# Kernel optimization log

Hardware: AMD Instinct MI355X
Metric: run time of the kernel (lower is better)

Reference implementation:

```python
import jax, jax.numpy as jnp
import numpy as np

# dims: L = 1 + H*W tokens (cls first), BT = B*T clips*frames
L, BT, D = 577, 128, 768
B, T = 16, 8
H = W = 24
CM = 192   # d_middle = D // REDUCTION(4)
CR = 48    # CM // rf_r(4)
K = 3      # rf_k and spatial kernel


def setup_inputs() -> dict:
    key = jax.random.key(0)
    ks = jax.random.split(key, 10)
    return {
        "x":      jax.random.normal(ks[0], (L, BT, D), jnp.float32),
        # tada_pre_proj: Linear(D -> CM)
        "w_pre":  jax.random.normal(ks[1], (D, CM), jnp.float32) * 0.02,
        "b_pre":  jnp.zeros((CM,), jnp.float32),
        # TAdaConv2dV2 base depthwise weight (1x3x3, groups=CM) and bias
        "w_base": jax.random.normal(ks[2], (K, K, 1, CM), jnp.float32) * 0.1,
        "b_conv": jnp.zeros((CM,), jnp.float32),
        # route function: global 1x1 branch, temporal conv a (CM->CR), temporal conv b (CR->CM, small init)
        "w_g":    jax.random.normal(ks[3], (CM, CM), jnp.float32) * 0.02,
        "b_g":    jnp.zeros((CM,), jnp.float32),
        "w_a":    jax.random.normal(ks[4], (K, CM, CR), jnp.float32) * 0.05,
        "b_a":    jnp.zeros((CR,), jnp.float32),
        "w_b":    jax.random.normal(ks[5], (K, CR, CM), jnp.float32) * 0.02,
        # tada_proj: Linear(CM -> D)
        "w_proj": jax.random.normal(ks[6], (CM, D), jnp.float32) * 0.02,
        "b_proj": jnp.zeros((D,), jnp.float32),
    }


def reference(x, w_pre, b_pre, w_base, b_conv, w_g, b_g, w_a, b_a, w_b, w_proj, b_proj):
    # --- tada_pre_proj ---
    h = x @ w_pre + b_pre                                   # [L, BT, CM]
    cls_tok, sp = h[:1], h[1:]                              # cls token bypasses the conv
    sp = sp.transpose(1, 0, 2).reshape(BT, H, W, CM)        # [BT, H, W, CM]

    # --- route function: per-frame, per-channel calibration alpha ---
    d = sp.reshape(B, T, H * W, CM).mean(axis=2)            # spatial avg pool -> [B, T, CM]
    g = d.mean(axis=1) @ w_g + b_g                          # global temporal descriptor [B, CM]
    a = jax.lax.conv_general_dilated(d + g[:, None, :], w_a, (1,), 'SAME',
                                     dimension_numbers=('NWC', 'WIO', 'NWC')) + b_a
    a = jax.nn.relu(a)                                      # [B, T, CR]
    alpha = jax.lax.conv_general_dilated(a, w_b, (1,), 'SAME',
                                         dimension_numbers=('NWC', 'WIO', 'NWC')) + 1.0  # [B, T, CM]

    # --- calibrated depthwise conv (cal_dim='cout') ---
    # conv2d(x, alpha * W_base) == alpha * conv2d(x, W_base) for depthwise cout calibration
    y = jax.lax.conv_general_dilated(sp, w_base, (1, 1), 'SAME',
                                     dimension_numbers=('NHWC', 'HWIO', 'NHWC'),
                                     feature_group_count=CM)
    y = y * alpha.reshape(BT, 1, 1, CM) + b_conv            # [BT, H, W, CM]
    y = y.reshape(BT, H * W, CM).transpose(1, 0, 2)         # [HW, BT, CM]
    out = jnp.concatenate([cls_tok, y], axis=0)             # [L, BT, CM]

    # --- QuickGELU + tada_proj ---
    out = out * jax.nn.sigmoid(1.702 * out)
    return out @ w_proj + b_proj                            # [L, BT, D]
```

## Files before the change

kernel.cpp:

```cpp
#include <hip/hip_runtime.h>

#define DEV __device__ __forceinline__

typedef short bf16x8 __attribute__((ext_vector_type(8)));
typedef float f32x4  __attribute__((ext_vector_type(4)));
typedef unsigned short ushort_t;


DEV unsigned short f2bf(float f) {
  unsigned u = __float_as_uint(f);
  unsigned r = (u + 0x7fffu + ((u >> 16) & 1u)) >> 16;
  return (unsigned short)r;
}

DEV unsigned cvt_pk_bf16(float a, float b) {
  unsigned r;
  asm("v_cvt_pk_bf16_f32 %0, %1, %2" : "=v"(r) : "v"(a), "v"(b));
  return r;
}

DEV float bf2f(unsigned short b) { return __uint_as_float((unsigned)b << 16); }

DEV float silu_g(float v) { return v / (1.f + __expf(-1.702f * v)); }

DEV void gload_lds16(const void* g, void* l) {
  __builtin_amdgcn_global_load_lds(
      (const __attribute__((address_space(1))) unsigned int*)g,
      (__attribute__((address_space(3))) unsigned int*)l, 16, 0, 0);
}

__global__ __launch_bounds__(256)
void prep_kernel(const float* __restrict__ w_pre, const float* __restrict__ w_proj,
                 short* __restrict__ w_preT, short* __restrict__ w_projT) {
  int i = blockIdx.x * 256 + threadIdx.x;
  if (i < 192 * 768) {
    int n = i / 768, k = i - n * 768;
    w_preT[i] = (short)f2bf(w_pre[k * 192 + n]);
    int n2 = i / 192, k2 = i - n2 * 192;
    w_projT[i] = (short)f2bf(w_proj[k2 * 768 + n2]);
  }
}

__global__ __launch_bounds__(512, 4)
void gemm1_kernel(const float* __restrict__ Af, const short* __restrict__ Bt,
                  const float* __restrict__ bias, ushort_t* __restrict__ C) {
  constexpr int BM = 128, BK = 64, KTOT = 768, NTOT = 192, NT = 12;
  __shared__ short As[2][BM * BK];
  __shared__ short Bs[2][192 * BK];

  const int tid  = threadIdx.x;
  const int wave = tid >> 6, lane = tid & 63;
  const int m0 = blockIdx.x * BM;
  const int wm = wave >> 2, wn = wave & 3;
  const int lr  = lane & 15;
  const int lk8 = lane >> 4;
  const int srow = lane >> 3;
  const int schunk = lane & 7;

  f32x4 acc[4][3] = {};
  float4 areg[2][2];

  auto loadA_f32 = [&](int kt) {
    #pragma unroll
    for (int s = 0; s < 2; ++s) {
      int id = tid + s * 512;
      int r = id >> 3, c = id & 7;
      int cg = c ^ (r & 7);
      const float* p = Af + (size_t)(m0 + r) * KTOT + kt + cg * 8;
      areg[s][0] = *(const float4*)p;
      areg[s][1] = *(const float4*)(p + 4);
    }
  };
  auto cvtStoreA = [&](int buf) {
    #pragma unroll
    for (int s = 0; s < 2; ++s) {
      int id = tid + s * 512;
      int r = id >> 3, c = id & 7;
      int4 w;
      w.x = (int)cvt_pk_bf16(areg[s][0].x, areg[s][0].y);
      w.y = (int)cvt_pk_bf16(areg[s][0].z, areg[s][0].w);
      w.z = (int)cvt_pk_bf16(areg[s][1].x, areg[s][1].y);
      w.w = (int)cvt_pk_bf16(areg[s][1].z, areg[s][1].w);
      *(int4*)&As[buf][r * 64 + c * 8] = w;
    }
  };
  auto stageB = [&](int kt, int buf) {
    #pragma unroll
    for (int j = 0; j < 3; ++j) {
      int rb8 = wave * 3 + j;
      int r = rb8 * 8 + srow;
      const short* src = Bt + (size_t)r * KTOT + kt + (schunk ^ srow) * 8;
      gload_lds16(src, (char*)Bs[buf] + rb8 * 1024);
    }
  };
  auto compute = [&](int buf) {
    #pragma unroll
    for (int ks = 0; ks < 2; ++ks) {
      int kc = ks * 4 + lk8;
      bf16x8 af[4], bfv[3];
      #pragma unroll
      for (int fm = 0; fm < 4; ++fm) {
        int row = wm * 64 + fm * 16 + lr;
        af[fm] = *(const bf16x8*)&As[buf][row * 64 + (kc ^ (row & 7)) * 8];
      }
      #pragma unroll
      for (int fn = 0; fn < 3; ++fn) {
        int row = wn * 48 + fn * 16 + lr;
        bfv[fn] = *(const bf16x8*)&Bs[buf][row * 64 + (kc ^ (row & 7)) * 8];
      }
      #pragma unroll
      for (int fm = 0; fm < 4; ++fm)
        #pragma unroll
        for (int fn = 0; fn < 3; ++fn)
          acc[fm][fn] = __builtin_amdgcn_mfma_f32_16x16x32_bf16(
              bfv[fn], af[fm], acc[fm][fn], 0, 0, 0);
    }
  };

  loadA_f32(0);
  cvtStoreA(0);
  stageB(0, 0);
  loadA_f32(BK);
  asm volatile("s_waitcnt vmcnt(4) lgkmcnt(0)" ::: "memory");
  __builtin_amdgcn_s_barrier();

  #pragma unroll
  for (int t = 0; t < NT; ++t) {
    const int cur = t & 1, nxt = cur ^ 1;
    if (t + 1 < NT) {
      stageB((t + 1) * BK, nxt);
      cvtStoreA(nxt);
      if (t + 2 < NT) loadA_f32((t + 2) * BK);
    }
    compute(cur);
    if (t + 1 < NT) {
      if (t + 2 < NT)
        asm volatile("s_waitcnt vmcnt(4) lgkmcnt(0)" ::: "memory");
      else
        asm volatile("s_waitcnt vmcnt(0) lgkmcnt(0)" ::: "memory");
      __builtin_amdgcn_s_barrier();
    }
  }

  const int cb = (lane >> 4) * 4;
  #pragma unroll
  for (int fm = 0; fm < 4; ++fm) {
    int row = m0 + wm * 64 + fm * 16 + lr;
    #pragma unroll
    for (int fn = 0; fn < 3; ++fn) {
      int col = wn * 48 + fn * 16 + cb;
      float4 bv = *(const float4*)(bias + col);
      int2 w;
      w.x = (int)cvt_pk_bf16(acc[fm][fn][0] + bv.x, acc[fm][fn][1] + bv.y);
      w.y = (int)cvt_pk_bf16(acc[fm][fn][2] + bv.z, acc[fm][fn][3] + bv.w);
      *(int2*)&C[(size_t)row * NTOT + col] = w;
    }
  }
}

__global__ __launch_bounds__(384)
void reduce_d_kernel(const ushort_t* __restrict__ h, float* __restrict__ d) {
  const int bt = blockIdx.x, tid = threadIdx.x;
  const int slice = tid / 24, c8 = tid % 24;
  __shared__ float part[16][192];
  float sum[8] = {};
  #pragma unroll 4
  for (int i = 0; i < 36; ++i) {
    int l = 1 + slice * 36 + i;
    bf16x8 v = *(const bf16x8*)&h[((size_t)l * 128 + bt) * 192 + c8 * 8];
    #pragma unroll
    for (int j = 0; j < 8; ++j) sum[j] += bf2f((unsigned short)v[j]);
  }
  #pragma unroll
  for (int j = 0; j < 8; ++j) part[slice][c8 * 8 + j] = sum[j];
  __syncthreads();
  if (tid < 192) {
    float s = 0.f;
    #pragma unroll
    for (int sl = 0; sl < 16; ++sl) s += part[sl][tid];
    d[bt * 192 + tid] = s * (1.f / 576.f);
  }
}

__global__ __launch_bounds__(256)
void small_path_kernel(const float* __restrict__ d,
                       const float* __restrict__ w_g, const float* __restrict__ b_g,
                       const float* __restrict__ w_a, const float* __restrict__ b_a,
                       const float* __restrict__ w_b,
                       float* __restrict__ alpha) {
  const int b = blockIdx.x, tid = threadIdx.x;
  __shared__ unsigned short wg_buf[36864];
  __shared__ unsigned short wa_buf[27648];
  __shared__ float e[8][192];
  __shared__ float md[192];
  __shared__ float a[8][48];

  #pragma unroll
  for (int it = 0; it < 36; ++it) {
    int i = tid + it * 256;
    float4 v = *(const float4*)(w_g + i * 4);
    int2 w;
    w.x = (int)cvt_pk_bf16(v.x, v.y);
    w.y = (int)cvt_pk_bf16(v.z, v.w);
    *(int2*)&wg_buf[i * 4] = w;
  }
  #pragma unroll
  for (int it = 0; it < 27; ++it) {
    int i = tid + it * 256;
    float4 v = *(const float4*)(w_a + i * 4);
    int2 w;
    w.x = (int)cvt_pk_bf16(v.x, v.y);
    w.y = (int)cvt_pk_bf16(v.z, v.w);
    *(int2*)&wa_buf[i * 4] = w;
  }
  for (int i = tid; i < 384; i += 256)
    *(float4*)((float*)e + i * 4) = *(const float4*)(d + (size_t)b * 1536 + i * 4);
  __syncthreads();

  if (tid < 192) {
    float m = 0.f;
    #pragma unroll
    for (int t = 0; t < 8; ++t) m += e[t][tid];
    md[tid] = m * 0.125f;
  }
  __syncthreads();

  if (tid < 192) {
    float accg = b_g[tid];
    #pragma unroll 8
    for (int k = 0; k < 192; ++k)
      accg += md[k] * bf2f(wg_buf[k * 192 + tid]);
    #pragma unroll
    for (int t = 0; t < 8; ++t) e[t][tid] += accg;
  }
  __syncthreads();

  #pragma unroll
  for (int it = 0; it < 27; ++it) {
    int i = tid + it * 256;
    float4 v = *(const float4*)(w_b + i * 4);
    int2 w;
    w.x = (int)cvt_pk_bf16(v.x, v.y);
    w.y = (int)cvt_pk_bf16(v.z, v.w);
    *(int2*)&wg_buf[i * 4] = w;
  }
  for (int o = tid; o < 384; o += 256) {
    int t = o / 48, r = o - t * 48;
    float acc = b_a[r];
    #pragma unroll
    for (int dt = 0; dt < 3; ++dt) {
      int tt = t + dt - 1;
      if ((unsigned)tt < 8u) {
        #pragma unroll 8
        for (int k = 0; k < 192; ++k)
          acc += e[tt][k] * bf2f(wa_buf[(dt * 192 + k) * 48 + r]);
      }
    }
    a[t][r] = fmaxf(acc, 0.f);
  }
  __syncthreads();

  if (tid < 192) {
    #pragma unroll
    for (int t = 0; t < 8; ++t) {
      float acc = 1.0f;
      #pragma unroll
      for (int dt = 0; dt < 3; ++dt) {
        int tt = t + dt - 1;
        if ((unsigned)tt < 8u) {
          #pragma unroll 8
          for (int r = 0; r < 48; ++r)
            acc += a[tt][r] * bf2f(wg_buf[(dt * 48 + r) * 192 + tid]);
        }
      }
      alpha[(size_t)(b * 8 + t) * 192 + tid] = acc;
    }
  }
}

__global__ __launch_bounds__(512, 4)
void fused_out_kernel(const ushort_t* __restrict__ h, const float* __restrict__ alpha,
                      const float* __restrict__ w_base, const float* __restrict__ b_conv,
                      const short* __restrict__ Bt, const float* __restrict__ bias,
                      float* __restrict__ out) {
  constexpr int NTOT = 768;
  __shared__ ushort_t Stile[64 * 192];

  const int tid  = threadIdx.x;
  const int l    = blockIdx.x >> 1;
  const int bt0  = (blockIdx.x & 1) * 64;
  const int wave = tid >> 6, lane = tid & 63;
  const int wm = wave >> 2, wn = wave & 3;
  const int lr = lane & 15, lk8 = lane >> 4;

  const int row = tid >> 3;
  const int cg  = tid & 7;
  const int bt  = bt0 + row;
  if (l == 0) {
    #pragma unroll
    for (int j = 0; j < 3; ++j) {
      int c8 = cg + 8 * j;
      bf16x8 hv = *(const bf16x8*)&h[(size_t)bt * 192 + c8 * 8];
      float v0 = silu_g(bf2f((ushort_t)hv[0])), v1 = silu_g(bf2f((ushort_t)hv[1]));
      float v2 = silu_g(bf2f((ushort_t)hv[2])), v3 = silu_g(bf2f((ushort_t)hv[3]));
      float v4 = silu_g(bf2f((ushort_t)hv[4])), v5 = silu_g(bf2f((ushort_t)hv[5]));
      float v6 = silu_g(bf2f((ushort_t)hv[6])), v7 = silu_g(bf2f((ushort_t)hv[7]));
      int4 pk;
      pk.x = (int)cvt_pk_bf16(v0, v1); pk.y = (int)cvt_pk_bf16(v2, v3);
      pk.z = (int)cvt_pk_bf16(v4, v5); pk.w = (int)cvt_pk_bf16(v6, v7);
      int chp = (c8 & ~7) | ((c8 & 7) ^ (row & 7));
      *(int4*)&Stile[row * 192 + chp * 8] = pk;
    }
  } else {
    const int p = l - 1, hh = p / 24, ww = p - hh * 24;
    #pragma unroll
    for (int j = 0; j < 3; ++j) {
      int c8 = cg + 8 * j;
      int cbase = c8 * 8;
      float acc8[8] = {};
      #pragma unroll
      for (int dh = 0; dh < 3; ++dh) {
        int y = hh + dh - 1;
        if ((unsigned)y >= 24u) continue;
        #pragma unroll
        for (int dw = 0; dw < 3; ++dw) {
          int xx = ww + dw - 1;
          if ((unsigned)xx >= 24u) continue;
          bf16x8 hv = *(const bf16x8*)
              &h[((size_t)(1 + y * 24 + xx) * 128 + bt) * 192 + cbase];
          const float* wp = w_base + (dh * 3 + dw) * 192 + cbase;
          float4 w0 = *(const float4*)wp, w1 = *(const float4*)(wp + 4);
          acc8[0] += bf2f((ushort_t)hv[0]) * w0.x;
          acc8[1] += bf2f((ushort_t)hv[1]) * w0.y;
          acc8[2] += bf2f((ushort_t)hv[2]) * w0.z;
          acc8[3] += bf2f((ushort_t)hv[3]) * w0.w;
          acc8[4] += bf2f((ushort_t)hv[4]) * w1.x;
          acc8[5] += bf2f((ushort_t)hv[5]) * w1.y;
          acc8[6] += bf2f((ushort_t)hv[6]) * w1.z;
          acc8[7] += bf2f((ushort_t)hv[7]) * w1.w;
        }
      }
      const float* ap = alpha + (size_t)bt * 192 + cbase;
      float4 a0 = *(const float4*)ap, a1 = *(const float4*)(ap + 4);
      const float* bp = b_conv + cbase;
      float4 c0 = *(const float4*)bp, c1 = *(const float4*)(bp + 4);
      float v0 = silu_g(acc8[0] * a0.x + c0.x), v1 = silu_g(acc8[1] * a0.y + c0.y);
      float v2 = silu_g(acc8[2] * a0.z + c0.z), v3 = silu_g(acc8[3] * a0.w + c0.w);
      float v4 = silu_g(acc8[4] * a1.x + c1.x), v5 = silu_g(acc8[5] * a1.y + c1.y);
      float v6 = silu_g(acc8[6] * a1.z + c1.z), v7 = silu_g(acc8[7] * a1.w + c1.w);
      int4 pk;
      pk.x = (int)cvt_pk_bf16(v0, v1); pk.y = (int)cvt_pk_bf16(v2, v3);
      pk.z = (int)cvt_pk_bf16(v4, v5); pk.w = (int)cvt_pk_bf16(v6, v7);
      int chp = (c8 & ~7) | ((c8 & 7) ^ (row & 7));
      *(int4*)&Stile[row * 192 + chp * 8] = pk;
    }
  }
  __syncthreads();

  bf16x8 areg[6][2];
  #pragma unroll
  for (int kt = 0; kt < 6; ++kt) {
    #pragma unroll
    for (int fm = 0; fm < 2; ++fm) {
      int sr = wm * 32 + fm * 16 + lr;
      int kc = kt * 4 + lk8;
      int chp = (kc & ~7) | ((kc & 7) ^ (sr & 7));
      areg[kt][fm] = *(const bf16x8*)&Stile[sr * 192 + chp * 8];
    }
  }

  const int cb = (lane >> 4) * 4;
  #pragma unroll 1
  for (int nc = 0; nc < 4; ++nc) {
    const int n0 = nc * 192;
    f32x4 acc[2][3] = {};
    #pragma unroll
    for (int kt = 0; kt < 6; ++kt) {
      bf16x8 bfv[3];
      #pragma unroll
      for (int fn = 0; fn < 3; ++fn)
        bfv[fn] = *(const bf16x8*)(Bt +
            (size_t)(n0 + wn * 48 + fn * 16 + lr) * 192 + kt * 32 + lk8 * 8);
      #pragma unroll
      for (int fm = 0; fm < 2; ++fm)
        #pragma unroll
        for (int fn = 0; fn < 3; ++fn)
          acc[fm][fn] = __builtin_amdgcn_mfma_f32_16x16x32_bf16(
              bfv[fn], areg[kt][fm], acc[fm][fn], 0, 0, 0);
    }
    #pragma unroll
    for (int fm = 0; fm < 2; ++fm) {
      int orow = l * 128 + bt0 + wm * 32 + fm * 16 + lr;
      #pragma unroll
      for (int fn = 0; fn < 3; ++fn) {
        int col = n0 + wn * 48 + fn * 16 + cb;
        float4 bv = *(const float4*)(bias + col);
        f32x4 o;
        o[0] = acc[fm][fn][0] + bv.x;
        o[1] = acc[fm][fn][1] + bv.y;
        o[2] = acc[fm][fn][2] + bv.z;
        o[3] = acc[fm][fn][3] + bv.w;
        *(f32x4*)&out[(size_t)orow * NTOT + col] = o;
      }
    }
  }
}

extern "C" void kernel_launch(void* const* d_in, const int* in_sizes, int n_in,
                              void* d_out, int out_size, void* d_ws, size_t ws_size,
                              hipStream_t stream) {
  (void)in_sizes; (void)n_in; (void)out_size; (void)ws_size;
  const float* x      = (const float*)d_in[0];
  const float* w_pre  = (const float*)d_in[1];
  const float* b_pre  = (const float*)d_in[2];
  const float* w_base = (const float*)d_in[3];
  const float* b_conv = (const float*)d_in[4];
  const float* w_g    = (const float*)d_in[5];
  const float* b_g    = (const float*)d_in[6];
  const float* w_a    = (const float*)d_in[7];
  const float* b_a    = (const float*)d_in[8];
  const float* w_b    = (const float*)d_in[9];
  const float* w_proj = (const float*)d_in[10];
  const float* b_proj = (const float*)d_in[11];

  float* out = (float*)d_out;
  char* ws = (char*)d_ws;
  short* w_preT  = (short*)(ws);
  short* w_projT = (short*)(ws + 294912);
  float* dbuf    = (float*)(ws + 589824);
  float* alpha   = (float*)(ws + 688128);
  ushort_t* h    = (ushort_t*)(ws + 786432);

  prep_kernel<<<576, 256, 0, stream>>>(w_pre, w_proj, w_preT, w_projT);

  gemm1_kernel<<<577, 512, 0, stream>>>(x, w_preT, b_pre, h);

  reduce_d_kernel<<<128, 384, 0, stream>>>(h, dbuf);
  small_path_kernel<<<16, 256, 0, stream>>>(dbuf, w_g, b_g, w_a, b_a, w_b, alpha);

  fused_out_kernel<<<1154, 512, 0, stream>>>(h, alpha, w_base, b_conv,
                                             w_projT, b_proj, out);
}
```

Baseline: 273.7 us.

## Retile fused output kernel to 16-row blocks with LDS-staged coalesced stores

Shrinks each block of the fused depthwise-conv + projection kernel from 64 to 16 token rows, giving four times as many blocks. Each wave now covers 96 output columns in a single pass. Results are staged through a shared float buffer and written with coalesced nontemporal stores. Interior pixels get a fast path that issues all nine neighbor loads without bounds checks. The aim is more parallelism, better store coalescing and more memory-level parallelism in the conv, at the cost of re-reading the projection weights four times as often per output row and using more LDS per block.

```diff
diff --git a/kernel.cpp b/kernel.cpp
--- a/kernel.cpp
+++ b/kernel.cpp
@@ -283,126 +283,135 @@
                       const float* __restrict__ w_base, const float* __restrict__ b_conv,
                       const short* __restrict__ Bt, const float* __restrict__ bias,
                       float* __restrict__ out) {
-  constexpr int NTOT = 768;
-  __shared__ ushort_t Stile[64 * 192];
+  __shared__ ushort_t Stile[16 * 192];
+  __shared__ float Obuf[16][772];
 
   const int tid  = threadIdx.x;
-  const int l    = blockIdx.x >> 1;
-  const int bt0  = (blockIdx.x & 1) * 64;
+  const int l    = blockIdx.x >> 3;
+  const int bt0  = (blockIdx.x & 7) * 16;
   const int wave = tid >> 6, lane = tid & 63;
-  const int wm = wave >> 2, wn = wave & 3;
   const int lr = lane & 15, lk8 = lane >> 4;
 
-  const int row = tid >> 3;
-  const int cg  = tid & 7;
-  const int bt  = bt0 + row;
-  if (l == 0) {
-    #pragma unroll
-    for (int j = 0; j < 3; ++j) {
-      int c8 = cg + 8 * j;
-      bf16x8 hv = *(const bf16x8*)&h[(size_t)bt * 192 + c8 * 8];
-      float v0 = silu_g(bf2f((ushort_t)hv[0])), v1 = silu_g(bf2f((ushort_t)hv[1]));
-      float v2 = silu_g(bf2f((ushort_t)hv[2])), v3 = silu_g(bf2f((ushort_t)hv[3]));
-      float v4 = silu_g(bf2f((ushort_t)hv[4])), v5 = silu_g(bf2f((ushort_t)hv[5]));
-      float v6 = silu_g(bf2f((ushort_t)hv[6])), v7 = silu_g(bf2f((ushort_t)hv[7]));
-      int4 pk;
-      pk.x = (int)cvt_pk_bf16(v0, v1); pk.y = (int)cvt_pk_bf16(v2, v3);
-      pk.z = (int)cvt_pk_bf16(v4, v5); pk.w = (int)cvt_pk_bf16(v6, v7);
-      int chp = (c8 & ~7) | ((c8 & 7) ^ (row & 7));
-      *(int4*)&Stile[row * 192 + chp * 8] = pk;
-    }
-  } else {
-    const int p = l - 1, hh = p / 24, ww = p - hh * 24;
-    #pragma unroll
-    for (int j = 0; j < 3; ++j) {
-      int c8 = cg + 8 * j;
-      int cbase = c8 * 8;
+  if (tid < 384) {
+    const int bt_i = tid / 24, c8 = tid - (tid / 24) * 24;
+    const int bt = bt0 + bt_i, cbase = c8 * 8;
+    float v[8];
+    if (l == 0) {
+      bf16x8 hv = *(const bf16x8*)&h[(size_t)bt * 192 + cbase];
+      #pragma unroll
+      for (int j = 0; j < 8; ++j) v[j] = silu_g(bf2f((ushort_t)hv[j]));
+    } else {
+      const int p = l - 1, hh = p / 24, ww = p - hh * 24;
       float acc8[8] = {};
-      #pragma unroll
-      for (int dh = 0; dh < 3; ++dh) {
-        int y = hh + dh - 1;
-        if ((unsigned)y >= 24u) continue;
+      const bool interior = (hh > 0) & (hh < 23) & (ww > 0) & (ww < 23);
+      if (interior) {
+        bf16x8 hv[9];
         #pragma unroll
-        for (int dw = 0; dw < 3; ++dw) {
-          int xx = ww + dw - 1;
-          if ((unsigned)xx >= 24u) continue;
-          bf16x8 hv = *(const bf16x8*)
-              &h[((size_t)(1 + y * 24 + xx) * 128 + bt) * 192 + cbase];
-          const float* wp = w_base + (dh * 3 + dw) * 192 + cbase;
+        for (int dh = 0; dh < 3; ++dh)
+          #pragma unroll
+          for (int dw = 0; dw < 3; ++dw)
+            hv[dh * 3 + dw] = *(const bf16x8*)
+                &h[((size_t)(1 + (hh + dh - 1) * 24 + (ww + dw - 1)) * 128 + bt) * 192 + cbase];
+        #pragma unroll
+        for (int t9 = 0; t9 < 9; ++t9) {
+          const float* wp = w_base + t9 * 192 + cbase;
           float4 w0 = *(const float4*)wp, w1 = *(const float4*)(wp + 4);
-          acc8[0] += bf2f((ushort_t)hv[0]) * w0.x;
-          acc8[1] += bf2f((ushort_t)hv[1]) * w0.y;
-          acc8[2] += bf2f((ushort_t)hv[2]) * w0.z;
-          acc8[3] += bf2f((ushort_t)hv[3]) * w0.w;
-          acc8[4] += bf2f((ushort_t)hv[4]) * w1.x;
-          acc8[5] += bf2f((ushort_t)hv[5]) * w1.y;
-          acc8[6] += bf2f((ushort_t)hv[6]) * w1.z;
-          acc8[7] += bf2f((ushort_t)hv[7]) * w1.w;
+          acc8[0] += bf2f((ushort_t)hv[t9][0]) * w0.x;
+          acc8[1] += bf2f((ushort_t)hv[t9][1]) * w0.y;
+          acc8[2] += bf2f((ushort_t)hv[t9][2]) * w0.z;
+          acc8[3] += bf2f((ushort_t)hv[t9][3]) * w0.w;
+          acc8[4] += bf2f((ushort_t)hv[t9][4]) * w1.x;
+          acc8[5] += bf2f((ushort_t)hv[t9][5]) * w1.y;
+          acc8[6] += bf2f((ushort_t)hv[t9][6]) * w1.z;
+          acc8[7] += bf2f((ushort_t)hv[t9][7]) * w1.w;
+        }
+      } else {
+        #pragma unroll
+        for (int dh = 0; dh < 3; ++dh) {
+          int y = hh + dh - 1;
+          if ((unsigned)y >= 24u) continue;
+          #pragma unroll
+          for (int dw = 0; dw < 3; ++dw) {
+            int xx = ww + dw - 1;
+            if ((unsigned)xx >= 24u) continue;
+            bf16x8 hv = *(const bf16x8*)
+                &h[((size_t)(1 + y * 24 + xx) * 128 + bt) * 192 + cbase];
+            const float* wp = w_base + (dh * 3 + dw) * 192 + cbase;
+            float4 w0 = *(const float4*)wp, w1 = *(const float4*)(wp + 4);
+            acc8[0] += bf2f((ushort_t)hv[0]) * w0.x;
+            acc8[1] += bf2f((ushort_t)hv[1]) * w0.y;
+            acc8[2] += bf2f((ushort_t)hv[2]) * w0.z;
+            acc8[3] += bf2f((ushort_t)hv[3]) * w0.w;
+            acc8[4] += bf2f((ushort_t)hv[4]) * w1.x;
+            acc8[5] += bf2f((ushort_t)hv[5]) * w1.y;
+            acc8[6] += bf2f((ushort_t)hv[6]) * w1.z;
+            acc8[7] += bf2f((ushort_t)hv[7]) * w1.w;
+          }
         }
       }
       const float* ap = alpha + (size_t)bt * 192 + cbase;
       float4 a0 = *(const float4*)ap, a1 = *(const float4*)(ap + 4);
       const float* bp = b_conv + cbase;
       float4 c0 = *(const float4*)bp, c1 = *(const float4*)(bp + 4);
-      float v0 = silu_g(acc8[0] * a0.x + c0.x), v1 = silu_g(acc8[1] * a0.y + c0.y);
-      float v2 = silu_g(acc8[2] * a0.z + c0.z), v3 = silu_g(acc8[3] * a0.w + c0.w);
-      float v4 = silu_g(acc8[4] * a1.x + c1.x), v5 = silu_g(acc8[5] * a1.y + c1.y);
-      float v6 = silu_g(acc8[6] * a1.z + c1.z), v7 = silu_g(acc8[7] * a1.w + c1.w);
-      int4 pk;
-      pk.x = (int)cvt_pk_bf16(v0, v1); pk.y = (int)cvt_pk_bf16(v2, v3);
-      pk.z = (int)cvt_pk_bf16(v4, v5); pk.w = (int)cvt_pk_bf16(v6, v7);
-      int chp = (c8 & ~7) | ((c8 & 7) ^ (row & 7));
-      *(int4*)&Stile[row * 192 + chp * 8] = pk;
-    }
-  }
-  __syncthreads();
-
-  bf16x8 areg[6][2];
+      v[0] = silu_g(acc8[0] * a0.x + c0.x);
+      v[1] = silu_g(acc8[1] * a0.y + c0.y);
+      v[2] = silu_g(acc8[2] * a0.z + c0.z);
+      v[3] = silu_g(acc8[3] * a0.w + c0.w);
+      v[4] = silu_g(acc8[4] * a1.x + c1.x);
+      v[5] = silu_g(acc8[5] * a1.y + c1.y);
+      v[6] = silu_g(acc8[6] * a1.z + c1.z);
+      v[7] = silu_g(acc8[7] * a1.w + c1.w);
+    }
+    int4 pk;
+    pk.x = (int)cvt_pk_bf16(v[0], v[1]); pk.y = (int)cvt_pk_bf16(v[2], v[3]);
+    pk.z = (int)cvt_pk_bf16(v[4], v[5]); pk.w = (int)cvt_pk_bf16(v[6], v[7]);
+    int chp = (c8 & ~7) | ((c8 & 7) ^ (bt_i & 7));
+    *(int4*)&Stile[bt_i * 192 + chp * 8] = pk;
+  }
+  __syncthreads();
+
+  const int colw = wave * 96;
+  bf16x8 af[6];
   #pragma unroll
   for (int kt = 0; kt < 6; ++kt) {
-    #pragma unroll
-    for (int fm = 0; fm < 2; ++fm) {
-      int sr = wm * 32 + fm * 16 + lr;
-      int kc = kt * 4 + lk8;
-      int chp = (kc & ~7) | ((kc & 7) ^ (sr & 7));
-      areg[kt][fm] = *(const bf16x8*)&Stile[sr * 192 + chp * 8];
-    }
-  }
-
-  const int cb = (lane >> 4) * 4;
-  #pragma unroll 1
-  for (int nc = 0; nc < 4; ++nc) {
-    const int n0 = nc * 192;
-    f32x4 acc[2][3] = {};
-    #pragma unroll
-    for (int kt = 0; kt < 6; ++kt) {
-      bf16x8 bfv[3];
-      #pragma unroll
-      for (int fn = 0; fn < 3; ++fn)
-        bfv[fn] = *(const bf16x8*)(Bt +
-            (size_t)(n0 + wn * 48 + fn * 16 + lr) * 192 + kt * 32 + lk8 * 8);
-      #pragma unroll
-      for (int fm = 0; fm < 2; ++fm)
-        #pragma unroll
-        for (int fn = 0; fn < 3; ++fn)
-          acc[fm][fn] = __builtin_amdgcn_mfma_f32_16x16x32_bf16(
-              bfv[fn], areg[kt][fm], acc[fm][fn], 0, 0, 0);
-    }
-    #pragma unroll
-    for (int fm = 0; fm < 2; ++fm) {
-      int orow = l * 128 + bt0 + wm * 32 + fm * 16 + lr;
-      #pragma unroll
-      for (int fn = 0; fn < 3; ++fn) {
-        int col = n0 + wn * 48 + fn * 16 + cb;
-        float4 bv = *(const float4*)(bias + col);
-        f32x4 o;
-        o[0] = acc[fm][fn][0] + bv.x;
-        o[1] = acc[fm][fn][1] + bv.y;
-        o[2] = acc[fm][fn][2] + bv.z;
-        o[3] = acc[fm][fn][3] + bv.w;
-        *(f32x4*)&out[(size_t)orow * NTOT + col] = o;
-      }
-    }
+    int kc = kt * 4 + lk8;
+    int chp = (kc & ~7) | ((kc & 7) ^ (lr & 7));
+    af[kt] = *(const bf16x8*)&Stile[lr * 192 + chp * 8];
+  }
+  f32x4 acc[6] = {};
+  #pragma unroll
+  for (int kt = 0; kt < 6; ++kt) {
+    bf16x8 bfv[6];
+    #pragma unroll
+    for (int fn = 0; fn < 6; ++fn)
+      bfv[fn] = *(const bf16x8*)(Bt +
+          (size_t)(colw + fn * 16 + lr) * 192 + kt * 32 + lk8 * 8);
+    #pragma unroll
+    for (int fn = 0; fn < 6; ++fn)
+      acc[fn] = __builtin_amdgcn_mfma_f32_16x16x32_bf16(
+          bfv[fn], af[kt], acc[fn], 0, 0, 0);
+  }
+  const int cb = lk8 * 4;
+  #pragma unroll
+  for (int fn = 0; fn < 6; ++fn) {
+    int col = colw + fn * 16 + cb;
+    float4 bv = *(const float4*)(bias + col);
+    f32x4 o;
+    o[0] = acc[fn][0] + bv.x;
+    o[1] = acc[fn][1] + bv.y;
+    o[2] = acc[fn][2] + bv.z;
+    o[3] = acc[fn][3] + bv.w;
+    *(f32x4*)&Obuf[lr][col] = o;
+  }
+  __syncthreads();
+
+  const size_t base = (size_t)(l * 128 + bt0) * 768;
+  #pragma unroll
+  for (int i = 0; i < 6; ++i) {
+    int v4 = i * 512 + tid;
+    int r = v4 / 192, c4 = v4 - r * 192;
+    f32x4 o = *(const f32x4*)&Obuf[r][c4 * 4];
+    __builtin_nontemporal_store(o, (f32x4*)&out[base + (size_t)r * 768 + c4 * 4]);
   }
 }
 
@@ -438,6 +447,6 @@
   reduce_d_kernel<<<128, 384, 0, stream>>>(h, dbuf);
   small_path_kernel<<<16, 256, 0, stream>>>(dbuf, w_g, b_g, w_a, b_a, w_b, alpha);
 
-  fused_out_kernel<<<1154, 512, 0, stream>>>(h, alpha, w_base, b_conv,
+  fused_out_kernel<<<4616, 512, 0, stream>>>(h, alpha, w_base, b_conv,
                                              w_projT, b_proj, out);
 }
```

New measurement: 297.0 us. 8.5% more time.
